# Performance work log

Measured on AMD Instinct MI355X. Metric: run time of the kernel, lower is better.

Reference implementation:

```python
import jax, jax.numpy as jnp
import numpy as np

E = 128       # embedding_size
H = 4         # num_heads
D = E // H    # head_dim = 32
PAD = 16      # window_size; full window width = 2*PAD+1 = 33
B = 4
N = 8192


def setup_inputs() -> dict:
    key = jax.random.key(0)
    ks = jax.random.split(key, 9)
    s = 1.0 / np.sqrt(E)
    return {
        "q": jax.random.normal(ks[0], (B, N, E), dtype=jnp.float32),
        "Wq_w": jax.random.normal(ks[1], (E, E), dtype=jnp.float32) * s,
        "Wq_b": jax.random.normal(ks[2], (E,), dtype=jnp.float32) * s,
        "Wk_w": jax.random.normal(ks[3], (E, E), dtype=jnp.float32) * s,
        "Wk_b": jax.random.normal(ks[4], (E,), dtype=jnp.float32) * s,
        "Wv_w": jax.random.normal(ks[5], (E, E), dtype=jnp.float32) * s,
        "Wv_b": jax.random.normal(ks[6], (E,), dtype=jnp.float32) * s,
        "Wo_w": jax.random.normal(ks[7], (E, E), dtype=jnp.float32) * s,
        "Wo_b": jax.random.normal(ks[8], (E,), dtype=jnp.float32) * s,
    }


def reference(q, Wq_w, Wq_b, Wk_w, Wk_b, Wv_w, Wv_b, Wo_w, Wo_b):
    # Self-attention: k = v = q (forward defaults).
    Q = q @ Wq_w.T + Wq_b
    K = q @ Wk_w.T + Wk_b
    V = q @ Wv_w.T + Wv_b
    b, n, _ = Q.shape
    # (b, H, n, D)
    Q = Q.reshape(b, n, H, D).transpose(0, 2, 1, 3)
    K = K.reshape(b, n, H, D).transpose(0, 2, 1, 3)
    V = V.reshape(b, n, H, D).transpose(0, 2, 1, 3)
    W = 2 * PAD + 1
    # Zero-pad the sequence dim (matches F.pad: padded keys are zero vectors,
    # included in softmax WITHOUT masking — faithful to the original).
    K_pad = jnp.pad(K, ((0, 0), (0, 0), (PAD, PAD), (0, 0)))
    V_pad = jnp.pad(V, ((0, 0), (0, 0), (PAD, PAD), (0, 0)))
    # Window gather indices: row n sees padded positions n .. n+2*PAD
    idx = jnp.arange(n)[:, None] + jnp.arange(W)[None, :]  # (n, W)
    K_win = K_pad[:, :, idx]  # (b, H, n, W, D)
    V_win = V_pad[:, :, idx]  # (b, H, n, W, D)
    scores = jnp.einsum("bhnd,bhnwd->bhnw", Q, K_win) / jnp.sqrt(
        jnp.asarray(D, dtype=Q.dtype)
    )
    probs = jax.nn.softmax(scores, axis=-1)  # dropout is identity in eval
    out = jnp.einsum("bhnw,bhnwd->bhnd", probs, V_win)
    out = out.transpose(0, 2, 1, 3).reshape(b, n, E)
    out = out @ Wo_w.T + Wo_b
    return out, probs
```

## Files before the change

kernel.cpp:

```cpp
#include <hip/hip_runtime.h>

#define BN 4
#define NN 8192
#define EE 128
#define HH 4
#define DD 32
#define WW 33
#define MROWS (BN*NN)
#define QELEMS (MROWS*EE)
#define WELEMS (EE*EE)

typedef __bf16 bf16x8 __attribute__((ext_vector_type(8)));
typedef float f32x4 __attribute__((ext_vector_type(4)));
typedef unsigned short u16x8 __attribute__((ext_vector_type(8)));

static __device__ __forceinline__ unsigned short f2bf(float x){
    unsigned u = __float_as_uint(x);
    u += 0x7fffu + ((u >> 16) & 1u);
    return (unsigned short)(u >> 16);
}
static __device__ __forceinline__ float bf2f(unsigned short h){
    return __uint_as_float(((unsigned)h) << 16);
}
static __device__ __forceinline__ bf16x8 ld_bf8(const unsigned short* p){
    u16x8 v = *(const u16x8*)p;
    return __builtin_bit_cast(bf16x8, v);
}

__global__ void __launch_bounds__(256) prep_w(const float* __restrict__ wq, const float* __restrict__ wk,
        const float* __restrict__ wv, const float* __restrict__ wo,
        unsigned short* __restrict__ wh, unsigned short* __restrict__ wl){
    int i = blockIdx.x*256 + threadIdx.x;
    int sel = i >> 14;
    const float* src = (sel==0)? wq : (sel==1)? wk : (sel==2)? wv : wo;
    float x = src[i & (WELEMS-1)];
    unsigned short h = f2bf(x);
    wh[i] = h;
    wl[i] = f2bf(x - bf2f(h));
}

__global__ void __launch_bounds__(256,4) gemm_qkv(const float* __restrict__ q,
        const unsigned short* __restrict__ wh, const unsigned short* __restrict__ wl,
        const float* __restrict__ bq, const float* __restrict__ bk, const float* __restrict__ bv_,
        float* __restrict__ Qf, float* __restrict__ Kf, float* __restrict__ Vf)
{
    const int wid = threadIdx.x >> 6;
    const int lane = threadIdx.x & 63;
    const int m = lane & 15, g = lane >> 4;
    const int row0 = blockIdx.x*64 + wid*16;
    const int ch = blockIdx.y;

    bf16x8 aH[4], aL[4];
    const float* qrow = q + (size_t)(row0 + m) * EE;
    #pragma unroll
    for (int kc=0;kc<4;kc++){
        float4 v0 = *(const float4*)(qrow + kc*32 + g*8);
        float4 v1 = *(const float4*)(qrow + kc*32 + g*8 + 4);
        float vv[8] = {v0.x,v0.y,v0.z,v0.w,v1.x,v1.y,v1.z,v1.w};
        u16x8 hh, ll;
        #pragma unroll
        for (int j=0;j<8;j++){
            unsigned short h = f2bf(vv[j]);
            hh[j] = h;
            ll[j] = f2bf(vv[j] - bf2f(h));
        }
        aH[kc] = __builtin_bit_cast(bf16x8, hh);
        aL[kc] = __builtin_bit_cast(bf16x8, ll);
    }

    const float* biases[3] = {bq, bk, bv_};
    float* outs[3] = {Qf, Kf, Vf};
    #pragma unroll
    for (int p=0;p<3;p++){
        const unsigned short* WH = wh + p*WELEMS;
        const unsigned short* WL = wl + p*WELEMS;
        const float* bias = biases[p];
        float* out = outs[p];
        #pragma unroll
        for (int cti=0; cti<4; cti++){
            const int col0 = (ch*4 + cti)*16;
            const size_t wbase = (size_t)(col0 + m) * EE;
            f32x4 acc = {0.f,0.f,0.f,0.f};
            #pragma unroll
            for (int kc=0;kc<4;kc++){
                bf16x8 bH = ld_bf8(WH + wbase + kc*32 + g*8);
                bf16x8 bL = ld_bf8(WL + wbase + kc*32 + g*8);
                acc = __builtin_amdgcn_mfma_f32_16x16x32_bf16(aH[kc], bH, acc, 0,0,0);
                acc = __builtin_amdgcn_mfma_f32_16x16x32_bf16(aH[kc], bL, acc, 0,0,0);
                acc = __builtin_amdgcn_mfma_f32_16x16x32_bf16(aL[kc], bH, acc, 0,0,0);
            }
            const float bv = bias[col0 + m];
            #pragma unroll
            for (int r=0;r<4;r++){
                int row = row0 + g*4 + r;
                out[(size_t)row*EE + col0 + m] = acc[r] + bv;
            }
        }
    }
}

__global__ void __launch_bounds__(256,4) gemm_o(const unsigned short* __restrict__ ah,
        const unsigned short* __restrict__ al,
        const unsigned short* __restrict__ WH, const unsigned short* __restrict__ WL,
        const float* __restrict__ bo, float* __restrict__ out)
{
    const int wid = threadIdx.x >> 6;
    const int lane = threadIdx.x & 63;
    const int m = lane & 15, g = lane >> 4;
    const int row0 = blockIdx.x*64 + wid*16;
    const int ch = blockIdx.y;

    bf16x8 aH[4], aL[4];
    const size_t abase = (size_t)(row0 + m) * EE;
    #pragma unroll
    for (int kc=0;kc<4;kc++){
        aH[kc] = ld_bf8(ah + abase + kc*32 + g*8);
        aL[kc] = ld_bf8(al + abase + kc*32 + g*8);
    }
    #pragma unroll
    for (int cti=0; cti<4; cti++){
        const int col0 = (ch*4 + cti)*16;
        const size_t wbase = (size_t)(col0 + m) * EE;
        f32x4 acc = {0.f,0.f,0.f,0.f};
        #pragma unroll
        for (int kc=0;kc<4;kc++){
            bf16x8 bH = ld_bf8(WH + wbase + kc*32 + g*8);
            bf16x8 bL = ld_bf8(WL + wbase + kc*32 + g*8);
            acc = __builtin_amdgcn_mfma_f32_16x16x32_bf16(aH[kc], bH, acc, 0,0,0);
            acc = __builtin_amdgcn_mfma_f32_16x16x32_bf16(aH[kc], bL, acc, 0,0,0);
            acc = __builtin_amdgcn_mfma_f32_16x16x32_bf16(aL[kc], bH, acc, 0,0,0);
        }
        const float bv = bo[col0 + m];
        #pragma unroll
        for (int r=0;r<4;r++){
            int row = row0 + g*4 + r;
            out[(size_t)row*EE + col0 + m] = acc[r] + bv;
        }
    }
}

__global__ void __launch_bounds__(256) attn_kernel(const float* __restrict__ Qf,
        const float* __restrict__ Kf, const float* __restrict__ Vf,
        float* __restrict__ probs, unsigned short* __restrict__ ah, unsigned short* __restrict__ al)
{
    __shared__ float Kl[96*33];
    __shared__ float Vl[96*33];
    __shared__ float Pl[64*WW];
    const int t = threadIdx.x;
    const int bh = blockIdx.y;
    const int b = bh >> 2, h = bh & 3;
    const int n0 = blockIdx.x * 64;
    const size_t rowbase = (size_t)b * NN;

    #pragma unroll
    for (int i=0;i<3;i++){
        int idx = t + i*256;
        int row = idx >> 3, q4 = idx & 7;
        int grow = n0 - 16 + row;
        float4 kv = make_float4(0.f,0.f,0.f,0.f);
        float4 vv = make_float4(0.f,0.f,0.f,0.f);
        if (grow >= 0 && grow < NN){
            size_t goff = (rowbase + grow)*EE + h*DD + q4*4;
            kv = *(const float4*)(Kf + goff);
            vv = *(const float4*)(Vf + goff);
        }
        int lo = row*33 + q4*4;
        *(float4*)(Kl + lo) = kv;
        *(float4*)(Vl + lo) = vv;
    }
    __syncthreads();

    const int p = t >> 2, e = t & 3;
    const int n = n0 + p;

    float qr[8];
    {
        const float4* qp = (const float4*)(Qf + (rowbase + n)*EE + h*DD + e*8);
        float4 v0 = qp[0], v1 = qp[1];
        qr[0]=v0.x; qr[1]=v0.y; qr[2]=v0.z; qr[3]=v0.w;
        qr[4]=v1.x; qr[5]=v1.y; qr[6]=v1.z; qr[7]=v1.w;
    }

    float sc[WW];
    #pragma unroll
    for (int w=0; w<WW; w++){
        const float* kr = &Kl[(p+w)*33 + e*8];
        float s = 0.f;
        #pragma unroll
        for (int k=0;k<8;k++) s = fmaf(qr[k], kr[k], s);
        sc[w] = s;
    }
    #pragma unroll
    for (int w=0; w<WW; w++){
        float s = sc[w];
        s += __shfl_xor(s, 1);
        s += __shfl_xor(s, 2);
        sc[w] = s * 0.17677669529663687f;
    }

    float mx = sc[0];
    #pragma unroll
    for (int w=1;w<WW;w++) mx = fmaxf(mx, sc[w]);
    float sum = 0.f;
    #pragma unroll
    for (int w=0;w<WW;w++){ sc[w] = __expf(sc[w]-mx); sum += sc[w]; }
    float inv = 1.f / sum;
    #pragma unroll
    for (int w=0;w<WW;w++) sc[w] *= inv;

    {
        float* pl = Pl + p*WW;
        if (e==0){
            #pragma unroll
            for (int w=0;w<9;w++) pl[w] = sc[w];
        } else if (e==1){
            #pragma unroll
            for (int w=9;w<17;w++) pl[w] = sc[w];
        } else if (e==2){
            #pragma unroll
            for (int w=17;w<25;w++) pl[w] = sc[w];
        } else {
            #pragma unroll
            for (int w=25;w<WW;w++) pl[w] = sc[w];
        }
    }

    float acc[8];
    #pragma unroll
    for (int k=0;k<8;k++) acc[k]=0.f;
    #pragma unroll
    for (int w=0;w<WW;w++){
        const float* vr = &Vl[(p+w)*33 + e*8];
        float pw = sc[w];
        #pragma unroll
        for (int k=0;k<8;k++) acc[k] = fmaf(pw, vr[k], acc[k]);
    }

    unsigned short hi[8], lo2[8];
    #pragma unroll
    for (int k=0;k<8;k++){ hi[k]=f2bf(acc[k]); lo2[k]=f2bf(acc[k]-bf2f(hi[k])); }
    size_t aoff = (rowbase + n)*EE + h*DD + e*8;
    *(ushort4*)(ah + aoff)     = make_ushort4(hi[0],hi[1],hi[2],hi[3]);
    *(ushort4*)(ah + aoff + 4) = make_ushort4(hi[4],hi[5],hi[6],hi[7]);
    *(ushort4*)(al + aoff)     = make_ushort4(lo2[0],lo2[1],lo2[2],lo2[3]);
    *(ushort4*)(al + aoff + 4) = make_ushort4(lo2[4],lo2[5],lo2[6],lo2[7]);

    __syncthreads();
    float* pbase = probs + ((size_t)bh*NN + n0)*WW;
    #pragma unroll
    for (int i=0;i<9;i++){
        int idx = t + i*256;
        if (idx < 64*WW) pbase[idx] = Pl[idx];
    }
}

extern "C" void kernel_launch(void* const* d_in, const int* in_sizes, int n_in,
                              void* d_out, int out_size, void* d_ws, size_t ws_size,
                              hipStream_t stream) {
    const float* q  = (const float*)d_in[0];
    const float* Wq = (const float*)d_in[1];  const float* bq = (const float*)d_in[2];
    const float* Wk = (const float*)d_in[3];  const float* bk = (const float*)d_in[4];
    const float* Wv = (const float*)d_in[5];  const float* bv = (const float*)d_in[6];
    const float* Wo = (const float*)d_in[7];  const float* bo = (const float*)d_in[8];

    float* out   = (float*)d_out;
    float* probs = out + QELEMS;

    unsigned short* a_hi = (unsigned short*)d_ws;
    unsigned short* a_lo = a_hi + QELEMS;
    unsigned short* w_hi = a_lo + QELEMS;
    unsigned short* w_lo = w_hi + 4*WELEMS;
    float* Qf = (float*)(w_lo + 4*WELEMS);
    float* Kf = Qf + QELEMS;
    float* Vf = Kf + QELEMS;

    prep_w<<<4*WELEMS/256, 256, 0, stream>>>(Wq, Wk, Wv, Wo, w_hi, w_lo);
    gemm_qkv<<<dim3(MROWS/64, 2), 256, 0, stream>>>(q, w_hi, w_lo,
                                                    bq, bk, bv, Qf, Kf, Vf);
    attn_kernel<<<dim3(NN/64, BN*HH), 256, 0, stream>>>(Qf, Kf, Vf, probs, a_hi, a_lo);
    gemm_o<<<dim3(MROWS/64, 2), 256, 0, stream>>>(a_hi, a_lo,
                                                  w_hi + 3*WELEMS, w_lo + 3*WELEMS, bo, out);
}
```

Baseline: 185.2 us.

## Keep weight fragments in registers and stream row tiles with prefetch

Both projection GEMMs are restructured so each of 8 waves owns a fixed 16-column slice of the output and loads its hi/lo bf16 weight fragments into registers once. A block then walks 8 row tiles of 16 rows, double-buffering the next tile's activation loads. This removes the repeated weight reloads per tile and the duplicate conversion of q into hi/lo for the two column-chunk blocks. The cost is higher register pressure (512 threads, 2 blocks per CU) and fewer blocks.

Result: faster. 161.7 us (-12.7%).

```diff
diff --git a/kernel.cpp b/kernel.cpp
--- a/kernel.cpp
+++ b/kernel.cpp
@@ -9,6 +9,7 @@
 #define MROWS (BN*NN)
 #define QELEMS (MROWS*EE)
 #define WELEMS (EE*EE)
+#define RT 8
 
 typedef __bf16 bf16x8 __attribute__((ext_vector_type(8)));
 typedef float f32x4 __attribute__((ext_vector_type(4)));
@@ -39,103 +40,133 @@
     wl[i] = f2bf(x - bf2f(h));
 }
 
-__global__ void __launch_bounds__(256,4) gemm_qkv(const float* __restrict__ q,
+__global__ void __launch_bounds__(512,2) gemm_qkv(const float* __restrict__ q,
         const unsigned short* __restrict__ wh, const unsigned short* __restrict__ wl,
         const float* __restrict__ bq, const float* __restrict__ bk, const float* __restrict__ bv_,
         float* __restrict__ Qf, float* __restrict__ Kf, float* __restrict__ Vf)
 {
-    const int wid = threadIdx.x >> 6;
+    const int w = threadIdx.x >> 6;
     const int lane = threadIdx.x & 63;
     const int m = lane & 15, g = lane >> 4;
-    const int row0 = blockIdx.x*64 + wid*16;
-    const int ch = blockIdx.y;
-
-    bf16x8 aH[4], aL[4];
-    const float* qrow = q + (size_t)(row0 + m) * EE;
-    #pragma unroll
-    for (int kc=0;kc<4;kc++){
-        float4 v0 = *(const float4*)(qrow + kc*32 + g*8);
-        float4 v1 = *(const float4*)(qrow + kc*32 + g*8 + 4);
-        float vv[8] = {v0.x,v0.y,v0.z,v0.w,v1.x,v1.y,v1.z,v1.w};
-        u16x8 hh, ll;
-        #pragma unroll
-        for (int j=0;j<8;j++){
-            unsigned short h = f2bf(vv[j]);
-            hh[j] = h;
-            ll[j] = f2bf(vv[j] - bf2f(h));
-        }
-        aH[kc] = __builtin_bit_cast(bf16x8, hh);
-        aL[kc] = __builtin_bit_cast(bf16x8, ll);
-    }
-
-    const float* biases[3] = {bq, bk, bv_};
-    float* outs[3] = {Qf, Kf, Vf};
-    #pragma unroll
-    for (int p=0;p<3;p++){
-        const unsigned short* WH = wh + p*WELEMS;
-        const unsigned short* WL = wl + p*WELEMS;
-        const float* bias = biases[p];
-        float* out = outs[p];
-        #pragma unroll
-        for (int cti=0; cti<4; cti++){
-            const int col0 = (ch*4 + cti)*16;
-            const size_t wbase = (size_t)(col0 + m) * EE;
+    const int rowB = blockIdx.x * (16*RT);
+
+    bf16x8 bH[3][4], bL[3][4];
+    #pragma unroll
+    for (int i=0;i<3;i++){
+        const unsigned short* WHp = wh + i*WELEMS + (size_t)(w*16 + m)*EE;
+        const unsigned short* WLp = wl + i*WELEMS + (size_t)(w*16 + m)*EE;
+        #pragma unroll
+        for (int kc=0;kc<4;kc++){
+            bH[i][kc] = ld_bf8(WHp + kc*32 + g*8);
+            bL[i][kc] = ld_bf8(WLp + kc*32 + g*8);
+        }
+    }
+    const float bias[3] = { bq[w*16+m], bk[w*16+m], bv_[w*16+m] };
+    float* const outp[3] = { Qf, Kf, Vf };
+
+    float4 fa[2][8];
+    {
+        const float* qrow = q + (size_t)(rowB + m) * EE;
+        #pragma unroll
+        for (int kc=0;kc<4;kc++){
+            fa[0][kc*2]   = *(const float4*)(qrow + kc*32 + g*8);
+            fa[0][kc*2+1] = *(const float4*)(qrow + kc*32 + g*8 + 4);
+        }
+    }
+    #pragma unroll
+    for (int rt=0; rt<RT; rt++){
+        const int row0 = rowB + rt*16;
+        if (rt+1 < RT){
+            const float* qrow = q + (size_t)(row0 + 16 + m) * EE;
+            #pragma unroll
+            for (int kc=0;kc<4;kc++){
+                fa[(rt+1)&1][kc*2]   = *(const float4*)(qrow + kc*32 + g*8);
+                fa[(rt+1)&1][kc*2+1] = *(const float4*)(qrow + kc*32 + g*8 + 4);
+            }
+        }
+        bf16x8 aH[4], aL[4];
+        #pragma unroll
+        for (int kc=0;kc<4;kc++){
+            float4 v0 = fa[rt&1][kc*2], v1 = fa[rt&1][kc*2+1];
+            float vv[8] = {v0.x,v0.y,v0.z,v0.w,v1.x,v1.y,v1.z,v1.w};
+            u16x8 hh, ll;
+            #pragma unroll
+            for (int j=0;j<8;j++){
+                unsigned short h = f2bf(vv[j]);
+                hh[j] = h;
+                ll[j] = f2bf(vv[j] - bf2f(h));
+            }
+            aH[kc] = __builtin_bit_cast(bf16x8, hh);
+            aL[kc] = __builtin_bit_cast(bf16x8, ll);
+        }
+        #pragma unroll
+        for (int i=0;i<3;i++){
             f32x4 acc = {0.f,0.f,0.f,0.f};
             #pragma unroll
             for (int kc=0;kc<4;kc++){
-                bf16x8 bH = ld_bf8(WH + wbase + kc*32 + g*8);
-                bf16x8 bL = ld_bf8(WL + wbase + kc*32 + g*8);
-                acc = __builtin_amdgcn_mfma_f32_16x16x32_bf16(aH[kc], bH, acc, 0,0,0);
-                acc = __builtin_amdgcn_mfma_f32_16x16x32_bf16(aH[kc], bL, acc, 0,0,0);
-                acc = __builtin_amdgcn_mfma_f32_16x16x32_bf16(aL[kc], bH, acc, 0,0,0);
+                acc = __builtin_amdgcn_mfma_f32_16x16x32_bf16(aH[kc], bH[i][kc], acc, 0,0,0);
+                acc = __builtin_amdgcn_mfma_f32_16x16x32_bf16(aH[kc], bL[i][kc], acc, 0,0,0);
+                acc = __builtin_amdgcn_mfma_f32_16x16x32_bf16(aL[kc], bH[i][kc], acc, 0,0,0);
             }
-            const float bv = bias[col0 + m];
-            #pragma unroll
-            for (int r=0;r<4;r++){
-                int row = row0 + g*4 + r;
-                out[(size_t)row*EE + col0 + m] = acc[r] + bv;
-            }
-        }
-    }
-}
-
-__global__ void __launch_bounds__(256,4) gemm_o(const unsigned short* __restrict__ ah,
+            float* op = outp[i] + (size_t)(row0 + g*4)*EE + w*16 + m;
+            #pragma unroll
+            for (int r=0;r<4;r++) op[(size_t)r*EE] = acc[r] + bias[i];
+        }
+    }
+}
+
+__global__ void __launch_bounds__(512,2) gemm_o(const unsigned short* __restrict__ ah,
         const unsigned short* __restrict__ al,
-        const unsigned short* __restrict__ WH, const unsigned short* __restrict__ WL,
+        const unsigned short* __restrict__ WHg, const unsigned short* __restrict__ WLg,
         const float* __restrict__ bo, float* __restrict__ out)
 {
-    const int wid = threadIdx.x >> 6;
+    const int w = threadIdx.x >> 6;
     const int lane = threadIdx.x & 63;
     const int m = lane & 15, g = lane >> 4;
-    const int row0 = blockIdx.x*64 + wid*16;
-    const int ch = blockIdx.y;
-
-    bf16x8 aH[4], aL[4];
-    const size_t abase = (size_t)(row0 + m) * EE;
-    #pragma unroll
-    for (int kc=0;kc<4;kc++){
-        aH[kc] = ld_bf8(ah + abase + kc*32 + g*8);
-        aL[kc] = ld_bf8(al + abase + kc*32 + g*8);
-    }
-    #pragma unroll
-    for (int cti=0; cti<4; cti++){
-        const int col0 = (ch*4 + cti)*16;
-        const size_t wbase = (size_t)(col0 + m) * EE;
+    const int rowB = blockIdx.x * (16*RT);
+
+    bf16x8 bH[4], bL[4];
+    {
+        const unsigned short* WHp = WHg + (size_t)(w*16 + m)*EE;
+        const unsigned short* WLp = WLg + (size_t)(w*16 + m)*EE;
+        #pragma unroll
+        for (int kc=0;kc<4;kc++){
+            bH[kc] = ld_bf8(WHp + kc*32 + g*8);
+            bL[kc] = ld_bf8(WLp + kc*32 + g*8);
+        }
+    }
+    const float biasv = bo[w*16+m];
+
+    bf16x8 fa[2][8];
+    {
+        const size_t abase = (size_t)(rowB + m) * EE;
+        #pragma unroll
+        for (int kc=0;kc<4;kc++){
+            fa[0][kc]   = ld_bf8(ah + abase + kc*32 + g*8);
+            fa[0][4+kc] = ld_bf8(al + abase + kc*32 + g*8);
+        }
+    }
+    #pragma unroll
+    for (int rt=0; rt<RT; rt++){
+        const int row0 = rowB + rt*16;
+        if (rt+1 < RT){
+            const size_t abase = (size_t)(row0 + 16 + m) * EE;
+            #pragma unroll
+            for (int kc=0;kc<4;kc++){
+                fa[(rt+1)&1][kc]   = ld_bf8(ah + abase + kc*32 + g*8);
+                fa[(rt+1)&1][4+kc] = ld_bf8(al + abase + kc*32 + g*8);
+            }
+        }
         f32x4 acc = {0.f,0.f,0.f,0.f};
         #pragma unroll
         for (int kc=0;kc<4;kc++){
-            bf16x8 bH = ld_bf8(WH + wbase + kc*32 + g*8);
-            bf16x8 bL = ld_bf8(WL + wbase + kc*32 + g*8);
-            acc = __builtin_amdgcn_mfma_f32_16x16x32_bf16(aH[kc], bH, acc, 0,0,0);
-            acc = __builtin_amdgcn_mfma_f32_16x16x32_bf16(aH[kc], bL, acc, 0,0,0);
-            acc = __builtin_amdgcn_mfma_f32_16x16x32_bf16(aL[kc], bH, acc, 0,0,0);
-        }
-        const float bv = bo[col0 + m];
-        #pragma unroll
-        for (int r=0;r<4;r++){
-            int row = row0 + g*4 + r;
-            out[(size_t)row*EE + col0 + m] = acc[r] + bv;
-        }
+            acc = __builtin_amdgcn_mfma_f32_16x16x32_bf16(fa[rt&1][kc],   bH[kc], acc, 0,0,0);
+            acc = __builtin_amdgcn_mfma_f32_16x16x32_bf16(fa[rt&1][kc],   bL[kc], acc, 0,0,0);
+            acc = __builtin_amdgcn_mfma_f32_16x16x32_bf16(fa[rt&1][4+kc], bH[kc], acc, 0,0,0);
+        }
+        float* op = out + (size_t)(row0 + g*4)*EE + w*16 + m;
+        #pragma unroll
+        for (int r=0;r<4;r++) op[(size_t)r*EE] = acc[r] + biasv;
     }
 }
 
@@ -275,9 +306,9 @@
     float* Vf = Kf + QELEMS;
 
     prep_w<<<4*WELEMS/256, 256, 0, stream>>>(Wq, Wk, Wv, Wo, w_hi, w_lo);
-    gemm_qkv<<<dim3(MROWS/64, 2), 256, 0, stream>>>(q, w_hi, w_lo,
-                                                    bq, bk, bv, Qf, Kf, Vf);
+    gemm_qkv<<<dim3(MROWS/(16*RT), 1), 512, 0, stream>>>(q, w_hi, w_lo,
+                                                         bq, bk, bv, Qf, Kf, Vf);
     attn_kernel<<<dim3(NN/64, BN*HH), 256, 0, stream>>>(Qf, Kf, Vf, probs, a_hi, a_lo);
-    gemm_o<<<dim3(MROWS/64, 2), 256, 0, stream>>>(a_hi, a_lo,
-                                                  w_hi + 3*WELEMS, w_lo + 3*WELEMS, bo, out);
-}
+    gemm_o<<<dim3(MROWS/(16*RT), 1), 512, 0, stream>>>(a_hi, a_lo,
+                                                       w_hi + 3*WELEMS, w_lo + 3*WELEMS, bo, out);
+}
```

## Restructure projection GEMMs with register-resident weights and prepped bf16 input

Applied to the files above, without the earlier changes.

Adds a prep_q kernel that splits q into bf16 hi/lo once, and replaces both projection GEMMs with one gemm_proj kernel. In it, each wave keeps a 32-column weight slice in registers and walks four 16-row tiles with double-buffered A loads, so weight reloads and repeated q conversion are avoided. The attention kernel reuses the K shared buffer for the probability staging, behind an extra barrier, to cut LDS use. The trade-offs are an extra pass over q through global memory, larger workspace, and higher register pressure (launch bounds lowered to 3).

Result: faster. 172.1 us (-7.1%).

```diff
diff --git a/kernel.cpp b/kernel.cpp
--- a/kernel.cpp
+++ b/kernel.cpp
@@ -25,6 +25,21 @@
 static __device__ __forceinline__ bf16x8 ld_bf8(const unsigned short* p){
     u16x8 v = *(const u16x8*)p;
     return __builtin_bit_cast(bf16x8, v);
+}
+
+__global__ void __launch_bounds__(256) prep_q(const float* __restrict__ q,
+        unsigned short* __restrict__ qh, unsigned short* __restrict__ ql){
+    int i = blockIdx.x*256 + threadIdx.x;
+    float4 v = ((const float4*)q)[i];
+    float vv[4] = {v.x, v.y, v.z, v.w};
+    unsigned short h[4], l[4];
+    #pragma unroll
+    for (int j=0;j<4;j++){
+        h[j] = f2bf(vv[j]);
+        l[j] = f2bf(vv[j] - bf2f(h[j]));
+    }
+    *(ushort4*)(qh + (size_t)i*4) = make_ushort4(h[0],h[1],h[2],h[3]);
+    *(ushort4*)(ql + (size_t)i*4) = make_ushort4(l[0],l[1],l[2],l[3]);
 }
 
 __global__ void __launch_bounds__(256) prep_w(const float* __restrict__ wq, const float* __restrict__ wk,
@@ -39,102 +54,68 @@
     wl[i] = f2bf(x - bf2f(h));
 }
 
-__global__ void __launch_bounds__(256,4) gemm_qkv(const float* __restrict__ q,
-        const unsigned short* __restrict__ wh, const unsigned short* __restrict__ wl,
-        const float* __restrict__ bq, const float* __restrict__ bk, const float* __restrict__ bv_,
-        float* __restrict__ Qf, float* __restrict__ Kf, float* __restrict__ Vf)
+__global__ void __launch_bounds__(256,3) gemm_proj(
+        const unsigned short* __restrict__ inh, const unsigned short* __restrict__ inl,
+        const unsigned short* __restrict__ whb, const unsigned short* __restrict__ wlb,
+        const float* __restrict__ b0, const float* __restrict__ b1, const float* __restrict__ b2,
+        float* __restrict__ o0, float* __restrict__ o1, float* __restrict__ o2)
 {
-    const int wid = threadIdx.x >> 6;
+    const int wv = threadIdx.x >> 6;
     const int lane = threadIdx.x & 63;
     const int m = lane & 15, g = lane >> 4;
-    const int row0 = blockIdx.x*64 + wid*16;
-    const int ch = blockIdx.y;
-
-    bf16x8 aH[4], aL[4];
-    const float* qrow = q + (size_t)(row0 + m) * EE;
-    #pragma unroll
-    for (int kc=0;kc<4;kc++){
-        float4 v0 = *(const float4*)(qrow + kc*32 + g*8);
-        float4 v1 = *(const float4*)(qrow + kc*32 + g*8 + 4);
-        float vv[8] = {v0.x,v0.y,v0.z,v0.w,v1.x,v1.y,v1.z,v1.w};
-        u16x8 hh, ll;
-        #pragma unroll
-        for (int j=0;j<8;j++){
-            unsigned short h = f2bf(vv[j]);
-            hh[j] = h;
-            ll[j] = f2bf(vv[j] - bf2f(h));
-        }
-        aH[kc] = __builtin_bit_cast(bf16x8, hh);
-        aL[kc] = __builtin_bit_cast(bf16x8, ll);
-    }
-
-    const float* biases[3] = {bq, bk, bv_};
-    float* outs[3] = {Qf, Kf, Vf};
-    #pragma unroll
-    for (int p=0;p<3;p++){
-        const unsigned short* WH = wh + p*WELEMS;
-        const unsigned short* WL = wl + p*WELEMS;
-        const float* bias = biases[p];
-        float* out = outs[p];
-        #pragma unroll
-        for (int cti=0; cti<4; cti++){
-            const int col0 = (ch*4 + cti)*16;
-            const size_t wbase = (size_t)(col0 + m) * EE;
+    const int y = blockIdx.y;
+    const int rowB = blockIdx.x * 64;
+
+    const unsigned short* WH = whb + (size_t)y*WELEMS;
+    const unsigned short* WL = wlb + (size_t)y*WELEMS;
+    const float* bias = (y==0)? b0 : (y==1)? b1 : b2;
+    float* outp = (y==0)? o0 : (y==1)? o1 : o2;
+
+    bf16x8 bH[2][4], bL[2][4];
+    #pragma unroll
+    for (int c=0;c<2;c++){
+        const unsigned short* WHp = WH + (size_t)(wv*32 + c*16 + m)*EE;
+        const unsigned short* WLp = WL + (size_t)(wv*32 + c*16 + m)*EE;
+        #pragma unroll
+        for (int kc=0;kc<4;kc++){
+            bH[c][kc] = ld_bf8(WHp + kc*32 + g*8);
+            bL[c][kc] = ld_bf8(WLp + kc*32 + g*8);
+        }
+    }
+    const float bias2[2] = { bias[wv*32+m], bias[wv*32+16+m] };
+
+    bf16x8 fa[2][8];
+    {
+        const size_t ab = (size_t)(rowB + m)*EE;
+        #pragma unroll
+        for (int kc=0;kc<4;kc++){
+            fa[0][kc]   = ld_bf8(inh + ab + kc*32 + g*8);
+            fa[0][4+kc] = ld_bf8(inl + ab + kc*32 + g*8);
+        }
+    }
+    #pragma unroll
+    for (int rt=0; rt<4; rt++){
+        const int row0 = rowB + rt*16;
+        if (rt < 3){
+            const size_t ab = (size_t)(row0 + 16 + m)*EE;
+            #pragma unroll
+            for (int kc=0;kc<4;kc++){
+                fa[(rt+1)&1][kc]   = ld_bf8(inh + ab + kc*32 + g*8);
+                fa[(rt+1)&1][4+kc] = ld_bf8(inl + ab + kc*32 + g*8);
+            }
+        }
+        #pragma unroll
+        for (int c=0;c<2;c++){
             f32x4 acc = {0.f,0.f,0.f,0.f};
             #pragma unroll
             for (int kc=0;kc<4;kc++){
-                bf16x8 bH = ld_bf8(WH + wbase + kc*32 + g*8);
-                bf16x8 bL = ld_bf8(WL + wbase + kc*32 + g*8);
-                acc = __builtin_amdgcn_mfma_f32_16x16x32_bf16(aH[kc], bH, acc, 0,0,0);
-                acc = __builtin_amdgcn_mfma_f32_16x16x32_bf16(aH[kc], bL, acc, 0,0,0);
-                acc = __builtin_amdgcn_mfma_f32_16x16x32_bf16(aL[kc], bH, acc, 0,0,0);
+                acc = __builtin_amdgcn_mfma_f32_16x16x32_bf16(fa[rt&1][kc],   bH[c][kc], acc, 0,0,0);
+                acc = __builtin_amdgcn_mfma_f32_16x16x32_bf16(fa[rt&1][kc],   bL[c][kc], acc, 0,0,0);
+                acc = __builtin_amdgcn_mfma_f32_16x16x32_bf16(fa[rt&1][4+kc], bH[c][kc], acc, 0,0,0);
             }
-            const float bv = bias[col0 + m];
-            #pragma unroll
-            for (int r=0;r<4;r++){
-                int row = row0 + g*4 + r;
-                out[(size_t)row*EE + col0 + m] = acc[r] + bv;
-            }
-        }
-    }
-}
-
-__global__ void __launch_bounds__(256,4) gemm_o(const unsigned short* __restrict__ ah,
-        const unsigned short* __restrict__ al,
-        const unsigned short* __restrict__ WH, const unsigned short* __restrict__ WL,
-        const float* __restrict__ bo, float* __restrict__ out)
-{
-    const int wid = threadIdx.x >> 6;
-    const int lane = threadIdx.x & 63;
-    const int m = lane & 15, g = lane >> 4;
-    const int row0 = blockIdx.x*64 + wid*16;
-    const int ch = blockIdx.y;
-
-    bf16x8 aH[4], aL[4];
-    const size_t abase = (size_t)(row0 + m) * EE;
-    #pragma unroll
-    for (int kc=0;kc<4;kc++){
-        aH[kc] = ld_bf8(ah + abase + kc*32 + g*8);
-        aL[kc] = ld_bf8(al + abase + kc*32 + g*8);
-    }
-    #pragma unroll
-    for (int cti=0; cti<4; cti++){
-        const int col0 = (ch*4 + cti)*16;
-        const size_t wbase = (size_t)(col0 + m) * EE;
-        f32x4 acc = {0.f,0.f,0.f,0.f};
-        #pragma unroll
-        for (int kc=0;kc<4;kc++){
-            bf16x8 bH = ld_bf8(WH + wbase + kc*32 + g*8);
-            bf16x8 bL = ld_bf8(WL + wbase + kc*32 + g*8);
-            acc = __builtin_amdgcn_mfma_f32_16x16x32_bf16(aH[kc], bH, acc, 0,0,0);
-            acc = __builtin_amdgcn_mfma_f32_16x16x32_bf16(aH[kc], bL, acc, 0,0,0);
-            acc = __builtin_amdgcn_mfma_f32_16x16x32_bf16(aL[kc], bH, acc, 0,0,0);
-        }
-        const float bv = bo[col0 + m];
-        #pragma unroll
-        for (int r=0;r<4;r++){
-            int row = row0 + g*4 + r;
-            out[(size_t)row*EE + col0 + m] = acc[r] + bv;
+            float* op = outp + (size_t)(row0 + g*4)*EE + wv*32 + c*16 + m;
+            #pragma unroll
+            for (int r=0;r<4;r++) op[(size_t)r*EE] = acc[r] + bias2[c];
         }
     }
 }
@@ -143,9 +124,8 @@
         const float* __restrict__ Kf, const float* __restrict__ Vf,
         float* __restrict__ probs, unsigned short* __restrict__ ah, unsigned short* __restrict__ al)
 {
-    __shared__ float Kl[96*33];
+    __shared__ float KP[96*33];
     __shared__ float Vl[96*33];
-    __shared__ float Pl[64*WW];
     const int t = threadIdx.x;
     const int bh = blockIdx.y;
     const int b = bh >> 2, h = bh & 3;
@@ -165,7 +145,7 @@
             vv = *(const float4*)(Vf + goff);
         }
         int lo = row*33 + q4*4;
-        *(float4*)(Kl + lo) = kv;
+        *(float4*)(KP + lo) = kv;
         *(float4*)(Vl + lo) = vv;
     }
     __syncthreads();
@@ -184,7 +164,7 @@
     float sc[WW];
     #pragma unroll
     for (int w=0; w<WW; w++){
-        const float* kr = &Kl[(p+w)*33 + e*8];
+        const float* kr = &KP[(p+w)*33 + e*8];
         float s = 0.f;
         #pragma unroll
         for (int k=0;k<8;k++) s = fmaf(qr[k], kr[k], s);
@@ -198,6 +178,8 @@
         sc[w] = s * 0.17677669529663687f;
     }
 
+    __syncthreads();
+
     float mx = sc[0];
     #pragma unroll
     for (int w=1;w<WW;w++) mx = fmaxf(mx, sc[w]);
@@ -209,7 +191,7 @@
     for (int w=0;w<WW;w++) sc[w] *= inv;
 
     {
-        float* pl = Pl + p*WW;
+        float* pl = KP + p*WW;
         if (e==0){
             #pragma unroll
             for (int w=0;w<9;w++) pl[w] = sc[w];
@@ -250,7 +232,7 @@
     #pragma unroll
     for (int i=0;i<9;i++){
         int idx = t + i*256;
-        if (idx < 64*WW) pbase[idx] = Pl[idx];
+        if (idx < 64*WW) pbase[idx] = KP[idx];
     }
 }
 
@@ -266,7 +248,9 @@
     float* out   = (float*)d_out;
     float* probs = out + QELEMS;
 
-    unsigned short* a_hi = (unsigned short*)d_ws;
+    unsigned short* q_hi = (unsigned short*)d_ws;
+    unsigned short* q_lo = q_hi + QELEMS;
+    unsigned short* a_hi = q_lo + QELEMS;
     unsigned short* a_lo = a_hi + QELEMS;
     unsigned short* w_hi = a_lo + QELEMS;
     unsigned short* w_lo = w_hi + 4*WELEMS;
@@ -274,10 +258,12 @@
     float* Kf = Qf + QELEMS;
     float* Vf = Kf + QELEMS;
 
+    prep_q<<<QELEMS/4/256, 256, 0, stream>>>(q, q_hi, q_lo);
     prep_w<<<4*WELEMS/256, 256, 0, stream>>>(Wq, Wk, Wv, Wo, w_hi, w_lo);
-    gemm_qkv<<<dim3(MROWS/64, 2), 256, 0, stream>>>(q, w_hi, w_lo,
-                                                    bq, bk, bv, Qf, Kf, Vf);
+    gemm_proj<<<dim3(MROWS/64, 3), 256, 0, stream>>>(q_hi, q_lo, w_hi, w_lo,
+                                                     bq, bk, bv, Qf, Kf, Vf);
     attn_kernel<<<dim3(NN/64, BN*HH), 256, 0, stream>>>(Qf, Kf, Vf, probs, a_hi, a_lo);
-    gemm_o<<<dim3(MROWS/64, 2), 256, 0, stream>>>(a_hi, a_lo,
-                                                  w_hi + 3*WELEMS, w_lo + 3*WELEMS, bo, out);
-}
+    gemm_proj<<<dim3(MROWS/64, 1), 256, 0, stream>>>(a_hi, a_lo,
+                                                     w_hi + 3*WELEMS, w_lo + 3*WELEMS,
+                                                     bo, bo, bo, out, out, out);
+}
```
